# Kernel optimization log

Measured on AMD Instinct MI355X. Metric: run time of the kernel, lower is better.

Reference implementation:

```python
import jax, jax.numpy as jnp
import numpy as np

N = 32768        # total nodes (B * max_num_nodes)
E = 524288       # edges, avg degree 16
F_ORI = 32       # data.x_ori feature dim
F_G = 32         # each gamora_output feature dim
IN = F_ORI + 3 * F_G  # 128
H = 256          # hidden_dim
OUT = 16         # out_dim
MAXN = 1024      # max_num_nodes
EPS = 1e-5       # BatchNorm eps


def setup_inputs() -> dict:
    key = jax.random.key(0)
    ks = list(jax.random.split(key, 32))
    g = lambda k, shape, fan: jax.random.normal(k, shape, jnp.float32) / np.sqrt(fan)
    inp = {}
    inp['x_ori'] = jax.random.normal(ks[0], (N, F_ORI), jnp.float32)
    inp['g0'] = jax.random.normal(ks[1], (N, F_G), jnp.float32)
    inp['g1'] = jax.random.normal(ks[2], (N, F_G), jnp.float32)
    inp['g2'] = jax.random.normal(ks[3], (N, F_G), jnp.float32)
    inp['edge_index'] = jax.random.randint(ks[4], (2, E), 0, N, jnp.int64)
    # SAGEConv layer 0: in_dim -> hidden
    inp['Wl0'] = g(ks[5], (IN, H), IN)
    inp['Wr0'] = g(ks[6], (IN, H), IN)
    inp['bb0'] = jnp.zeros((H,), jnp.float32)
    # SAGEConv layers 1..3: hidden -> hidden (stacked)
    inp['Wl'] = g(ks[7], (3, H, H), H)
    inp['Wr'] = g(ks[8], (3, H, H), H)
    inp['bb'] = jnp.zeros((3, H), jnp.float32)
    # BatchNorm per conv layer
    inp['gamma'] = jnp.ones((4, H), jnp.float32)
    inp['beta'] = jnp.zeros((4, H), jnp.float32)
    # mlp1: [max_num_nodes, hidden, 1]
    inp['W1a'] = g(ks[9], (MAXN, H), MAXN)
    inp['b1a'] = jnp.zeros((H,), jnp.float32)
    inp['W1b'] = g(ks[10], (H, 1), H)
    inp['b1b'] = jnp.zeros((1,), jnp.float32)
    # final BatchNorm
    inp['gamma_f'] = jnp.ones((H,), jnp.float32)
    inp['beta_f'] = jnp.zeros((H,), jnp.float32)
    # mlp2: [hidden, hidden, out_dim]
    inp['W2a'] = g(ks[11], (H, H), H)
    inp['b2a'] = jnp.zeros((H,), jnp.float32)
    inp['W2b'] = g(ks[12], (H, OUT), H)
    inp['b2b'] = jnp.zeros((OUT,), jnp.float32)
    return inp


def _bn(x, gamma, beta):
    # training-mode BatchNorm1d over the node/batch axis (biased variance)
    m = jnp.mean(x, axis=0)
    v = jnp.var(x, axis=0)
    return (x - m) * jax.lax.rsqrt(v + EPS) * gamma + beta


def _sage(x, src, dst, inv_deg, Wl, Wr, b):
    # mean neighbor aggregation (gather -> segment_sum -> normalize), then
    # out = lin_l(mean_agg) + lin_r(x)  (PyG SAGEConv, aggr='mean')
    agg = jax.ops.segment_sum(x[src], dst, num_segments=N)
    mean = agg * inv_deg[:, None]
    return mean @ Wl + x @ Wr + b


def reference(x_ori, g0, g1, g2, edge_index, Wl0, Wr0, bb0, Wl, Wr, bb,
              gamma, beta, W1a, b1a, W1b, b1b, gamma_f, beta_f,
              W2a, b2a, W2b, b2b):
    x = jnp.concatenate([x_ori, g0, g1, g2], axis=1)  # [N, IN]
    dst, src = edge_index[0], edge_index[1]
    deg = jax.ops.segment_sum(jnp.ones((E,), x.dtype), dst, num_segments=N)
    inv_deg = jnp.where(deg > 0, 1.0 / jnp.maximum(deg, 1.0), 0.0)
    # layer 0
    x = jax.nn.relu(_bn(_sage(x, src, dst, inv_deg, Wl0, Wr0, bb0), gamma[0], beta[0]))
    # layers 1..3 (dropout is identity in eval-mode reference)
    for i in range(3):
        x = jax.nn.relu(_bn(_sage(x, src, dst, inv_deg, Wl[i], Wr[i], bb[i]),
                            gamma[i + 1], beta[i + 1]))
    x = x.reshape(-1, H, MAXN)                 # [B, H, MAXN]
    h = jax.nn.relu(x @ W1a + b1a)             # [B, H, H]
    x = (h @ W1b + b1b).squeeze(2)             # [B, H]
    x = jax.nn.relu(_bn(x, gamma_f, beta_f))
    x = jax.nn.relu(x @ W2a + b2a) @ W2b + b2b  # [B, OUT]
    return x
```

## Files before the change

kernel.cpp:

```cpp
#include <hip/hip_runtime.h>

#define NN 32768
#define NE 524288
#define HD 256
#define TOTP 794897

#define GAS __attribute__((address_space(1)))
#define LAS __attribute__((address_space(3)))

typedef __attribute__((ext_vector_type(8))) __bf16 bf16x8;
typedef __attribute__((ext_vector_type(4))) float f32x4;

__device__ __forceinline__ float ld_any(const void* p, int i, int isbf16) {
    return isbf16 ? (float)((const __bf16*)p)[i] : ((const float*)p)[i];
}

struct PtrTable { const void* p[18]; };


__global__ __launch_bounds__(256) void k_pre(const unsigned* __restrict__ xw, const int* __restrict__ ei,
                                             PtrTable pt, const void* __restrict__ p0, const void* __restrict__ p1,
                                             const void* __restrict__ p2, const void* __restrict__ p3,
                                             int* __restrict__ flags, int* __restrict__ deg,
                                             __bf16* __restrict__ blob, __bf16* __restrict__ X0c) {
    __shared__ int fl[2];
    const int t = threadIdx.x;
    if (t < 64) {
        unsigned L = xw[t] & 0xFFFFu;
        int e = (int)((L >> 7) & 0xFF);
        unsigned long long b = __ballot(e >= 90 && e <= 135);
        if (t == 0) fl[0] = (b == ~0ULL) ? 1 : 0;
    } else if (t < 128) {
        int u = t - 64;
        unsigned long long b = __ballot(ei[2 * u + 1] != 0);
        if (t == 64) fl[1] = (b == 0ULL) ? 1 : 0;
    }
    __syncthreads();
    const int f0 = fl[0], f1 = fl[1];
    const int blk = blockIdx.x;
    if (blk == 0 && t < 2) flags[t] = fl[t];
    if (blk < 2048) {
        int i0 = (blk * 256 + t) * 8;
        int n = i0 >> 7, f = i0 & 127;
        const void* src = (f < 32) ? p0 : (f < 64) ? p1 : (f < 96) ? p2 : p3;
        int si = n * 32 + (f & 31);
        bf16x8 o;
        #pragma unroll
        for (int j = 0; j < 8; ++j) o[j] = (__bf16)ld_any(src, si + j, f0);
        *(bf16x8*)&X0c[i0] = o;
    } else if (blk < 3601) {
        const int off[23] = {0, 32768, 65536, 65792, 131328, 196864, 262400, 327936, 393472,
                             459008, 459776, 460800, 461824, 723968, 724224, 724480, 724481,
                             724737, 724993, 790529, 790785, 794881, TOTP};
        const signed char pidx[22] = {0, 1, 2, 3, 3, 3, 4, 4, 4, 5, 6, 7, 8, 9, 10, 11, 12, 13, 14, 15, 16, 17};
        const int sbase[22] = {0, 0, 0, 0, 65536, 131072, 0, 65536, 131072, 0, 0, 0, 0, 0, 0, 0, 0, 0, 0, 0, 0, 0};
        const signed char lR[22] = {7, 7, -1, 8, 8, 8, 8, 8, 8, -1, -1, -1, 10, -1, -1, -1, -1, -1, -1, -1, -1, -1};
        const signed char lC[22] = {8, 8, 0, 8, 8, 8, 8, 8, 8, 0, 0, 0, 8, 0, 0, 0, 0, 0, 0, 0, 0, 0};
        int base = ((blk - 2048) * 256 + t) * 2;
        #pragma unroll
        for (int j = 0; j < 2; ++j) {
            int i = base + j;
            if (i >= TOTP) break;
            int s = 0;
            while (i >= off[s + 1]) ++s;
            int jj = i - off[s];
            int si;
            if (lR[s] >= 0) {
                int Rm = (1 << lR[s]) - 1;
                si = sbase[s] + ((jj & Rm) << lC[s]) + (jj >> lR[s]);
            } else {
                si = sbase[s] + jj;
            }
            blob[i] = (__bf16)ld_any(pt.p[pidx[s]], si, f0);
        }
    } else {
        int e0 = ((blk - 3601) * 256 + t) * 2;
        int d0 = f1 ? ei[2 * e0] : ei[e0];
        int d1 = f1 ? ei[2 * e0 + 2] : ei[e0 + 1];
        atomicAdd(&deg[d0], 1);
        atomicAdd(&deg[d1], 1);
    }
}


__global__ __launch_bounds__(256) void k_alloc(const int* __restrict__ deg, int* __restrict__ gcur,
                                               int* __restrict__ offs, float* __restrict__ invd) {
    const int n = blockIdx.x * 256 + threadIdx.x;
    const int lane = threadIdx.x & 63;
    const int v = deg[n];
    invd[n] = v ? 1.f / (float)v : 0.f;
    int incl = v;
    #pragma unroll
    for (int d = 1; d < 64; d <<= 1) {
        int y = __shfl_up(incl, d, 64);
        if (lane >= d) incl += y;
    }
    int base = 0;
    if (lane == 63) base = atomicAdd(gcur, incl);
    base = __shfl(base, 63, 64);
    offs[n] = base + incl - v;
}

__global__ __launch_bounds__(256) void k_fill(const int* __restrict__ ei, const int* __restrict__ flags,
                                              const int* __restrict__ offs, int* __restrict__ cursor,
                                              int* __restrict__ csr) {
    int e = blockIdx.x * 256 + threadIdx.x;
    int f = flags[1];
    int d = f ? ei[2 * e] : ei[e];
    int s = f ? ei[2 * NE + 2 * e] : ei[NE + e];
    int p = atomicAdd(&cursor[d], 1);
    csr[offs[d] + p] = s;
}


__global__ __launch_bounds__(256) void k_agg0(const __bf16* __restrict__ X, const int* __restrict__ csr,
                                              const int* __restrict__ offs, const int* __restrict__ deg,
                                              const float* __restrict__ invd, __bf16* __restrict__ M) {
    const int t = threadIdx.x;
    const int s = blockIdx.x & 1;
    const int n = (blockIdx.x >> 1) * 32 + (t >> 3);
    const int fo = s * 64 + (t & 7) * 8;
    const int beg = offs[n], end = beg + deg[n];
    float a[8] = {};
    for (int e = beg; e < end; e += 8) {
        #pragma unroll
        for (int u = 0; u < 8; ++u) {
            int ee = e + u;
            int idx = csr[ee < end ? ee : end - 1] & (NN - 1);
            float mk = ee < end ? 1.f : 0.f;
            bf16x8 v = *(const bf16x8*)&X[(size_t)idx * 128 + fo];
            #pragma unroll
            for (int j = 0; j < 8; ++j) a[j] += mk * (float)v[j];
        }
    }
    const float id = invd[n];
    bf16x8 o;
    #pragma unroll
    for (int j = 0; j < 8; ++j) o[j] = (__bf16)(a[j] * id);
    *(bf16x8*)&M[(size_t)n * 128 + fo] = o;
}


__global__ __launch_bounds__(256) void k_aggbn(const __bf16* __restrict__ X, const int* __restrict__ csr,
                                               const int* __restrict__ offs, const int* __restrict__ deg,
                                               const float* __restrict__ invd, const float* __restrict__ pstat,
                                               const __bf16* __restrict__ gamma, const __bf16* __restrict__ beta,
                                               __bf16* __restrict__ M) {
    const int t = threadIdx.x;
    const int s = blockIdx.x & 3;
    const int n = (blockIdx.x >> 2) * 32 + (t >> 3);
    const int fo = s * 64 + (t & 7) * 8;
    float sc[8], sh[8];
    {
        const float invn = 1.0f / NN;
        #pragma unroll
        for (int j = 0; j < 8; ++j) {
            const int c = fo + j;
            float m = pstat[c] * invn;
            float var = fmaxf(pstat[256 + c] * invn - m * m, 0.f);
            float rs = rsqrtf(var + 1e-5f);
            float g = (float)gamma[c] * rs;
            sc[j] = g;
            sh[j] = (float)beta[c] - m * g;
        }
    }
    const int beg = offs[n], end = beg + deg[n];
    float a[8] = {};
    for (int e = beg; e < end; e += 8) {
        #pragma unroll
        for (int u = 0; u < 8; ++u) {
            int ee = e + u;
            int idx = csr[ee < end ? ee : end - 1] & (NN - 1);
            float mk = ee < end ? 1.f : 0.f;
            bf16x8 v = *(const bf16x8*)&X[(size_t)idx * HD + fo];
            #pragma unroll
            for (int j = 0; j < 8; ++j) a[j] += mk * fmaxf((float)v[j] * sc[j] + sh[j], 0.f);
        }
    }
    const float id = invd[n];
    bf16x8 o;
    #pragma unroll
    for (int j = 0; j < 8; ++j) o[j] = (__bf16)(a[j] * id);
    *(bf16x8*)&M[(size_t)n * HD + fo] = o;
}


template <int MODE, int TM, int BNA>
__global__ __launch_bounds__(256) void k_gemm(const __bf16* __restrict__ A1, const __bf16* __restrict__ WT1,
                                              const __bf16* __restrict__ A2, const __bf16* __restrict__ WT2,
                                              const __bf16* __restrict__ bias, int KD,
                                              __bf16* __restrict__ O, float* __restrict__ colsum,
                                              const __bf16* __restrict__ W1b, float* __restrict__ x2,
                                              const float* __restrict__ pstatA, const __bf16* __restrict__ gA,
                                              const __bf16* __restrict__ bA) {
    constexpr int MI = TM / 32;
    __shared__ __bf16 As[2][TM][32];
    __shared__ __bf16 Bs[2][128][32];
    __shared__ float scs[256], shs[256];
    const int t = threadIdx.x;
    const int lane = t & 63, w = t >> 6;
    const int wm = w >> 1, wn = w & 1;
    const int quad = lane >> 4, l15 = lane & 15;
    const int row0 = blockIdx.x * TM, c0 = blockIdx.y * 128;
    const int dr = lane >> 2, dc = (lane & 3) * 8;
    if constexpr (BNA != 0) {
        const float invn = 1.0f / NN;
        float m = pstatA[t] * invn;
        float var = fmaxf(pstatA[256 + t] * invn - m * m, 0.f);
        float rs = rsqrtf(var + 1e-5f);
        float g = (float)gA[t] * rs;
        scs[t] = g;
        shs[t] = (float)bA[t] - m * g;
    }
    f32x4 acc[MI][4] = {};
    const int npass = A2 ? 2 : 1;
    for (int pass = 0; pass < npass; ++pass) {
        const __bf16* __restrict__ A = pass ? A2 : A1;
        const __bf16* __restrict__ WT = pass ? WT2 : WT1;
        for (int k0 = 0; k0 < KD; k0 += 64) {
            __syncthreads();
            #pragma unroll
            for (int kk = 0; kk < 2; ++kk) {
                #pragma unroll
                for (int i = 0; i < 2; ++i) {
                    const __bf16* g = &WT[(size_t)(c0 + w * 32 + i * 16 + dr) * KD + k0 + kk * 32 + dc];
                    __builtin_amdgcn_global_load_lds((const GAS void*)g, (LAS void*)&Bs[kk][w * 32 + i * 16][0],
                                                     16, 0, 0);
                }
                if ((BNA >> pass) & 1) {
                    const int kb = (k0 + kk * 32 + dc) & 255;
                    #pragma unroll
                    for (int i = 0; i < TM / 64; ++i) {
                        const __bf16* g = &A[(size_t)(row0 + w * (TM / 4) + i * 16 + dr) * KD + k0 + kk * 32 + dc];
                        bf16x8 v = *(const bf16x8*)g;
                        bf16x8 o;
                        #pragma unroll
                        for (int j = 0; j < 8; ++j)
                            o[j] = (__bf16)fmaxf((float)v[j] * scs[kb + j] + shs[kb + j], 0.f);
                        *(bf16x8*)&As[kk][w * (TM / 4) + i * 16 + dr][dc] = o;
                    }
                } else {
                    #pragma unroll
                    for (int i = 0; i < TM / 64; ++i) {
                        const __bf16* g = &A[(size_t)(row0 + w * (TM / 4) + i * 16 + dr) * KD + k0 + kk * 32 + dc];
                        __builtin_amdgcn_global_load_lds((const GAS void*)g,
                                                         (LAS void*)&As[kk][w * (TM / 4) + i * 16 + dr][0], 16, 0, 0);
                    }
                }
            }
            __syncthreads();
            #pragma unroll
            for (int kk = 0; kk < 2; ++kk) {
                bf16x8 af[MI], bfr[4];
                #pragma unroll
                for (int i = 0; i < MI; ++i) af[i] = *(const bf16x8*)&As[kk][wm * (TM / 2) + i * 16 + l15][quad * 8];
                #pragma unroll
                for (int j = 0; j < 4; ++j) bfr[j] = *(const bf16x8*)&Bs[kk][wn * 64 + j * 16 + l15][quad * 8];
                #pragma unroll
                for (int i = 0; i < MI; ++i)
                    #pragma unroll
                    for (int j = 0; j < 4; ++j)
                        acc[i][j] = __builtin_amdgcn_mfma_f32_16x16x32_bf16(af[i], bfr[j], acc[i][j], 0, 0, 0);
            }
        }
    }
    __syncthreads();
    if constexpr (MODE == 0) {
        float* lsum = (float*)&As[0][0][0];
        lsum[t] = 0.f;
        __syncthreads();
        #pragma unroll
        for (int j = 0; j < 4; ++j) {
            const int cb = wn * 64 + j * 16 + l15;
            const int col = c0 + cb;
            const float b = (float)bias[col];
            float s = 0.f, q = 0.f;
            #pragma unroll
            for (int i = 0; i < MI; ++i) {
                const size_t rbase = (size_t)(row0 + wm * (TM / 2) + i * 16 + quad * 4) * HD + col;
                #pragma unroll
                for (int r = 0; r < 4; ++r) {
                    float y = acc[i][j][r] + b;
                    O[rbase + (size_t)r * HD] = (__bf16)y;
                    s += y;
                    q += y * y;
                }
            }
            s += __shfl_xor(s, 16, 64); s += __shfl_xor(s, 32, 64);
            q += __shfl_xor(q, 16, 64); q += __shfl_xor(q, 32, 64);
            if (quad == 0) {
                atomicAdd(&lsum[cb], s);
                atomicAdd(&lsum[128 + cb], q);
            }
        }
        __syncthreads();
        if (t < 128) atomicAdd(&colsum[c0 + t], lsum[t]);
        else atomicAdd(&colsum[256 + c0 + t - 128], lsum[t]);
    } else {
        float bj[4], wj[4];
        #pragma unroll
        for (int j = 0; j < 4; ++j) {
            const int col = c0 + wn * 64 + j * 16 + l15;
            bj[j] = (float)bias[col];
            wj[j] = (float)W1b[col];
        }
        #pragma unroll
        for (int i = 0; i < MI; ++i) {
            #pragma unroll
            for (int r = 0; r < 4; ++r) {
                float p = 0.f;
                #pragma unroll
                for (int j = 0; j < 4; ++j) p += fmaxf(acc[i][j][r] + bj[j], 0.f) * wj[j];
                p += __shfl_xor(p, 1, 64); p += __shfl_xor(p, 2, 64);
                p += __shfl_xor(p, 4, 64); p += __shfl_xor(p, 8, 64);
                if (l15 == 0) atomicAdd(&x2[row0 + wm * (TM / 2) + i * 16 + quad * 4 + r], p);
            }
        }
    }
}


__global__ __launch_bounds__(256) void k_mlp2(const float* __restrict__ x2, const __bf16* __restrict__ b1b,
                                              const __bf16* __restrict__ gf, const __bf16* __restrict__ bf_,
                                              const __bf16* __restrict__ W2a, const __bf16* __restrict__ b2a,
                                              const __bf16* __restrict__ W2b, const __bf16* __restrict__ b2b,
                                              const int* __restrict__ flags, void* __restrict__ out) {
    __shared__ float row[HD];
    __shared__ float hbuf[HD];
    __shared__ float part[256];
    const int b = blockIdx.x, t = threadIdx.x;
    const float b1 = (float)b1b[0];
    float s = 0.f, q = 0.f, mine = 0.f;
    #pragma unroll
    for (int r = 0; r < 32; ++r) {
        float v = x2[r * HD + t] + b1;
        s += v; q += v * v;
        if (r == b) mine = v;
    }
    float m = s * (1.0f / 32.0f);
    float var = fmaxf(q * (1.0f / 32.0f) - m * m, 0.f);
    float rs = rsqrtf(var + 1e-5f);
    float sc = (float)gf[t] * rs;
    float sh = (float)bf_[t] - m * sc;
    row[t] = fmaxf(mine * sc + sh, 0.f);
    __syncthreads();
    float acc = (float)b2a[t];
    for (int j = 0; j < HD; ++j) acc += row[j] * (float)W2a[j * HD + t];
    hbuf[t] = fmaxf(acc, 0.f);
    __syncthreads();
    const int k = t & 15, g = t >> 4;
    float p = 0.f;
    #pragma unroll
    for (int jj = 0; jj < 16; ++jj) p += hbuf[g * 16 + jj] * (float)W2b[(g * 16 + jj) * 16 + k];
    part[t] = p;
    __syncthreads();
    if (t < 16) {
        float o = (float)b2b[t];
        #pragma unroll
        for (int g2 = 0; g2 < 16; ++g2) o += part[g2 * 16 + t];
        if (flags[0]) ((__bf16*)out)[b * 16 + t] = (__bf16)o;
        else ((float*)out)[b * 16 + t] = o;
    }
}


extern "C" void kernel_launch(void* const* d_in, const int* in_sizes, int n_in,
                              void* d_out, int out_size, void* d_ws, size_t ws_size,
                              hipStream_t stream) {
    const int* ei = (const int*)d_in[4];

    char* ws = (char*)d_ws;
    size_t off_ = 0;
    auto ALLOC = [&](size_t b) { char* p = ws + off_; off_ += (b + 255) & ~(size_t)255; return p; };
    int* flags_ = (int*)ALLOC(8);
    size_t zbeg = off_;
    int* deg_ = (int*)ALLOC(NN * 4);
    int* cursor_ = (int*)ALLOC(NN * 4);
    float* colsum_ = (float*)ALLOC(4 * 512 * 4);
    float* x2_ = (float*)ALLOC(8192 * 4);
    int* gcur_ = (int*)ALLOC(4);
    size_t zlen = off_ - zbeg;
    int* offs_ = (int*)ALLOC(NN * 4);
    float* invd_ = (float*)ALLOC(NN * 4);
    int* csr_ = (int*)ALLOC((size_t)NE * 4);
    __bf16* blob_ = (__bf16*)ALLOC((size_t)TOTP * 2);
    __bf16* M_ = (__bf16*)ALLOC((size_t)NN * HD * 2);
    __bf16* Xa_ = (__bf16*)ALLOC((size_t)NN * HD * 2);
    __bf16* Xb_ = (__bf16*)ALLOC((size_t)NN * HD * 2);
    __bf16* X0c_ = Xb_;

    __bf16* Wl0T = blob_ + 0;
    __bf16* Wr0T = blob_ + 32768;
    __bf16* bb0c = blob_ + 65536;
    __bf16* WlT = blob_ + 65792;
    __bf16* WrT = blob_ + 262400;
    __bf16* bbc = blob_ + 459008;
    __bf16* gammac = blob_ + 459776;
    __bf16* betac = blob_ + 460800;
    __bf16* W1aT = blob_ + 461824;
    __bf16* b1ac = blob_ + 723968;
    __bf16* W1bc = blob_ + 724224;
    __bf16* b1bc = blob_ + 724480;
    __bf16* gfc = blob_ + 724481;
    __bf16* bfc = blob_ + 724737;
    __bf16* W2ac = blob_ + 724993;
    __bf16* b2ac = blob_ + 790529;
    __bf16* W2bc = blob_ + 790785;
    __bf16* b2bc = blob_ + 794881;

    PtrTable pt;
    pt.p[0] = d_in[5];  pt.p[1] = d_in[6];  pt.p[2] = d_in[7];  pt.p[3] = d_in[8];
    pt.p[4] = d_in[9];  pt.p[5] = d_in[10]; pt.p[6] = d_in[11]; pt.p[7] = d_in[12];
    pt.p[8] = d_in[13]; pt.p[9] = d_in[14]; pt.p[10] = d_in[15]; pt.p[11] = d_in[16];
    pt.p[12] = d_in[17]; pt.p[13] = d_in[18]; pt.p[14] = d_in[19]; pt.p[15] = d_in[20];
    pt.p[16] = d_in[21]; pt.p[17] = d_in[22];

    hipMemsetAsync(ws + zbeg, 0, zlen, stream);
    k_pre<<<4625, 256, 0, stream>>>((const unsigned*)d_in[0], ei, pt, d_in[0], d_in[1], d_in[2], d_in[3],
                                    flags_, deg_, blob_, X0c_);
    k_alloc<<<NN / 256, 256, 0, stream>>>(deg_, gcur_, offs_, invd_);
    k_fill<<<NE / 256, 256, 0, stream>>>(ei, flags_, offs_, cursor_, csr_);

    k_agg0<<<NN / 32 * 2, 256, 0, stream>>>(X0c_, csr_, offs_, deg_, invd_, M_);
    k_gemm<0, 128, 0><<<dim3(NN / 128, 2), 256, 0, stream>>>(M_, Wl0T, X0c_, Wr0T, bb0c, 128, Xa_, colsum_,
                                                             nullptr, nullptr, nullptr, nullptr, nullptr);

    __bf16* Xin = Xa_;
    __bf16* Xo = Xb_;
    for (int l = 0; l < 3; ++l) {
        float* csprev = colsum_ + l * 512;
        float* cs = colsum_ + (l + 1) * 512;
        k_aggbn<<<NN / 32 * 4, 256, 0, stream>>>(Xin, csr_, offs_, deg_, invd_, csprev,
                                                 gammac + l * HD, betac + l * HD, M_);
        k_gemm<0, 128, 2><<<dim3(NN / 128, 2), 256, 0, stream>>>(M_, WlT + (size_t)l * HD * HD, Xin,
                                                                 WrT + (size_t)l * HD * HD, bbc + l * HD, 256, Xo,
                                                                 cs, nullptr, nullptr, csprev,
                                                                 gammac + l * HD, betac + l * HD);
        __bf16* tmp = Xin; Xin = Xo; Xo = tmp;
    }

    k_gemm<1, 64, 1><<<dim3(8192 / 64, 2), 256, 0, stream>>>(Xin, W1aT, nullptr, nullptr, b1ac, 1024, nullptr,
                                                             nullptr, W1bc, x2_, colsum_ + 3 * 512,
                                                             gammac + 3 * HD, betac + 3 * HD);
    k_mlp2<<<32, 256, 0, stream>>>(x2_, b1bc, gfc, bfc, W2ac, b2ac, W2bc, b2bc, flags_, d_out);
}
```

Before: 442.3 us.

## Apply BatchNorm once per layer and degree-sort nodes for aggregation

```diff
diff --git a/kernel.cpp b/kernel.cpp
--- a/kernel.cpp
+++ b/kernel.cpp
@@ -84,11 +84,13 @@
 
 
 __global__ __launch_bounds__(256) void k_alloc(const int* __restrict__ deg, int* __restrict__ gcur,
-                                               int* __restrict__ offs, float* __restrict__ invd) {
+                                               int* __restrict__ offs, float* __restrict__ invd,
+                                               int* __restrict__ hist) {
     const int n = blockIdx.x * 256 + threadIdx.x;
     const int lane = threadIdx.x & 63;
     const int v = deg[n];
     invd[n] = v ? 1.f / (float)v : 0.f;
+    atomicAdd(&hist[v < 255 ? v : 255], 1);
     int incl = v;
     #pragma unroll
     for (int d = 1; d < 64; d <<= 1) {
@@ -99,6 +101,21 @@
     if (lane == 63) base = atomicAdd(gcur, incl);
     base = __shfl(base, 63, 64);
     offs[n] = base + incl - v;
+}
+
+__global__ void k_prefix(int* __restrict__ hist) {
+    if (threadIdx.x == 0) {
+        int s = 0;
+        for (int i = 0; i < 256; ++i) { int v = hist[i]; hist[i] = s; s += v; }
+    }
+}
+
+__global__ __launch_bounds__(256) void k_scatter(const int* __restrict__ deg, int* __restrict__ hist,
+                                                 int* __restrict__ perm) {
+    const int n = blockIdx.x * 256 + threadIdx.x;
+    const int v = deg[n];
+    const int p = atomicAdd(&hist[v < 255 ? v : 255], 1);
+    perm[p] = n;
 }
 
 __global__ __launch_bounds__(256) void k_fill(const int* __restrict__ ei, const int* __restrict__ flags,
@@ -115,10 +132,11 @@
 
 __global__ __launch_bounds__(256) void k_agg0(const __bf16* __restrict__ X, const int* __restrict__ csr,
                                               const int* __restrict__ offs, const int* __restrict__ deg,
-                                              const float* __restrict__ invd, __bf16* __restrict__ M) {
+                                              const float* __restrict__ invd, const int* __restrict__ perm,
+                                              __bf16* __restrict__ M) {
     const int t = threadIdx.x;
     const int s = blockIdx.x & 1;
-    const int n = (blockIdx.x >> 1) * 32 + (t >> 3);
+    const int n = perm[(blockIdx.x >> 1) * 32 + (t >> 3)];
     const int fo = s * 64 + (t & 7) * 8;
     const int beg = offs[n], end = beg + deg[n];
     float a[8] = {};
@@ -140,30 +158,14 @@
     *(bf16x8*)&M[(size_t)n * 128 + fo] = o;
 }
 
-
-__global__ __launch_bounds__(256) void k_aggbn(const __bf16* __restrict__ X, const int* __restrict__ csr,
-                                               const int* __restrict__ offs, const int* __restrict__ deg,
-                                               const float* __restrict__ invd, const float* __restrict__ pstat,
-                                               const __bf16* __restrict__ gamma, const __bf16* __restrict__ beta,
-                                               __bf16* __restrict__ M) {
+__global__ __launch_bounds__(256) void k_agg(const __bf16* __restrict__ X, const int* __restrict__ csr,
+                                             const int* __restrict__ offs, const int* __restrict__ deg,
+                                             const float* __restrict__ invd, const int* __restrict__ perm,
+                                             __bf16* __restrict__ M) {
     const int t = threadIdx.x;
     const int s = blockIdx.x & 3;
-    const int n = (blockIdx.x >> 2) * 32 + (t >> 3);
+    const int n = perm[(blockIdx.x >> 2) * 32 + (t >> 3)];
     const int fo = s * 64 + (t & 7) * 8;
-    float sc[8], sh[8];
-    {
-        const float invn = 1.0f / NN;
-        #pragma unroll
-        for (int j = 0; j < 8; ++j) {
-            const int c = fo + j;
-            float m = pstat[c] * invn;
-            float var = fmaxf(pstat[256 + c] * invn - m * m, 0.f);
-            float rs = rsqrtf(var + 1e-5f);
-            float g = (float)gamma[c] * rs;
-            sc[j] = g;
-            sh[j] = (float)beta[c] - m * g;
-        }
-    }
     const int beg = offs[n], end = beg + deg[n];
     float a[8] = {};
     for (int e = beg; e < end; e += 8) {
@@ -174,7 +176,7 @@
             float mk = ee < end ? 1.f : 0.f;
             bf16x8 v = *(const bf16x8*)&X[(size_t)idx * HD + fo];
             #pragma unroll
-            for (int j = 0; j < 8; ++j) a[j] += mk * fmaxf((float)v[j] * sc[j] + sh[j], 0.f);
+            for (int j = 0; j < 8; ++j) a[j] += mk * (float)v[j];
         }
     }
     const float id = invd[n];
@@ -320,6 +322,30 @@
 }
 
 
+__global__ __launch_bounds__(256) void k_bnapply(__bf16* __restrict__ Y, const float* __restrict__ pstat,
+                                                 const __bf16* __restrict__ gamma, const __bf16* __restrict__ beta) {
+    __shared__ float sc[256], sh[256];
+    const int t = threadIdx.x;
+    {
+        const float invn = 1.0f / NN;
+        float m = pstat[t] * invn;
+        float var = fmaxf(pstat[256 + t] * invn - m * m, 0.f);
+        float rs = rsqrtf(var + 1e-5f);
+        float s = (float)gamma[t] * rs;
+        sc[t] = s;
+        sh[t] = (float)beta[t] - m * s;
+    }
+    __syncthreads();
+    size_t i = ((size_t)blockIdx.x * 256 + t) * 8;
+    int c = (int)(i & 255);
+    bf16x8 y = *(const bf16x8*)&Y[i];
+    bf16x8 o;
+    #pragma unroll
+    for (int j = 0; j < 8; ++j) o[j] = (__bf16)fmaxf((float)y[j] * sc[c + j] + sh[c + j], 0.f);
+    *(bf16x8*)&Y[i] = o;
+}
+
+
 __global__ __launch_bounds__(256) void k_mlp2(const float* __restrict__ x2, const __bf16* __restrict__ b1b,
                                               const __bf16* __restrict__ gf, const __bf16* __restrict__ bf_,
                                               const __bf16* __restrict__ W2a, const __bf16* __restrict__ b2a,
@@ -379,9 +405,11 @@
     float* colsum_ = (float*)ALLOC(4 * 512 * 4);
     float* x2_ = (float*)ALLOC(8192 * 4);
     int* gcur_ = (int*)ALLOC(4);
+    int* hist_ = (int*)ALLOC(256 * 4);
     size_t zlen = off_ - zbeg;
     int* offs_ = (int*)ALLOC(NN * 4);
     float* invd_ = (float*)ALLOC(NN * 4);
+    int* perm_ = (int*)ALLOC(NN * 4);
     int* csr_ = (int*)ALLOC((size_t)NE * 4);
     __bf16* blob_ = (__bf16*)ALLOC((size_t)TOTP * 2);
     __bf16* M_ = (__bf16*)ALLOC((size_t)NN * HD * 2);
@@ -418,24 +446,25 @@
     hipMemsetAsync(ws + zbeg, 0, zlen, stream);
     k_pre<<<4625, 256, 0, stream>>>((const unsigned*)d_in[0], ei, pt, d_in[0], d_in[1], d_in[2], d_in[3],
                                     flags_, deg_, blob_, X0c_);
-    k_alloc<<<NN / 256, 256, 0, stream>>>(deg_, gcur_, offs_, invd_);
+    k_alloc<<<NN / 256, 256, 0, stream>>>(deg_, gcur_, offs_, invd_, hist_);
+    k_prefix<<<1, 64, 0, stream>>>(hist_);
+    k_scatter<<<NN / 256, 256, 0, stream>>>(deg_, hist_, perm_);
     k_fill<<<NE / 256, 256, 0, stream>>>(ei, flags_, offs_, cursor_, csr_);
 
-    k_agg0<<<NN / 32 * 2, 256, 0, stream>>>(X0c_, csr_, offs_, deg_, invd_, M_);
+    k_agg0<<<NN / 32 * 2, 256, 0, stream>>>(X0c_, csr_, offs_, deg_, invd_, perm_, M_);
     k_gemm<0, 128, 0><<<dim3(NN / 128, 2), 256, 0, stream>>>(M_, Wl0T, X0c_, Wr0T, bb0c, 128, Xa_, colsum_,
                                                              nullptr, nullptr, nullptr, nullptr, nullptr);
+    k_bnapply<<<NN / 8, 256, 0, stream>>>(Xa_, colsum_, gammac, betac);
 
     __bf16* Xin = Xa_;
     __bf16* Xo = Xb_;
     for (int l = 0; l < 3; ++l) {
-        float* csprev = colsum_ + l * 512;
         float* cs = colsum_ + (l + 1) * 512;
-        k_aggbn<<<NN / 32 * 4, 256, 0, stream>>>(Xin, csr_, offs_, deg_, invd_, csprev,
-                                                 gammac + l * HD, betac + l * HD, M_);
-        k_gemm<0, 128, 2><<<dim3(NN / 128, 2), 256, 0, stream>>>(M_, WlT + (size_t)l * HD * HD, Xin,
+        k_agg<<<NN / 32 * 4, 256, 0, stream>>>(Xin, csr_, offs_, deg_, invd_, perm_, M_);
+        k_gemm<0, 128, 0><<<dim3(NN / 128, 2), 256, 0, stream>>>(M_, WlT + (size_t)l * HD * HD, Xin,
                                                                  WrT + (size_t)l * HD * HD, bbc + l * HD, 256, Xo,
-                                                                 cs, nullptr, nullptr, csprev,
-                                                                 gammac + l * HD, betac + l * HD);
+                                                                 cs, nullptr, nullptr, nullptr, nullptr, nullptr);
+        if (l < 2) k_bnapply<<<NN / 8, 256, 0, stream>>>(Xo, cs, gammac + (l + 1) * HD, betac + (l + 1) * HD);
         __bf16* tmp = Xin; Xin = Xo; Xo = tmp;
     }
 
```

New measurement: 593.2 us. 1.34x slower.
